# Kernel optimization log

Hardware: AMD Instinct MI355X
Metric: run time of the kernel (lower is better)

Reference implementation:

```python
import jax, jax.numpy as jnp
import numpy as np
import math

N_VERT = 35709
N_FACE = 70789
BATCH = 32


def _normalize(x, axis=-1, eps=1e-12):
    n = jnp.linalg.norm(x, axis=axis, keepdims=True)
    return x / jnp.maximum(n, eps)


def setup_inputs() -> dict:
    key = jax.random.key(0)
    ks = jax.random.split(key, 9)
    coeff = jax.random.normal(ks[0], (BATCH, 277), jnp.float32)
    idBase = jax.random.normal(ks[1], (3 * N_VERT, 80), jnp.float32)
    exBase = jax.random.normal(ks[2], (3 * N_VERT, 64), jnp.float32)
    texBase = jax.random.normal(ks[3], (3 * N_VERT, 100), jnp.float32)
    meanshape = jax.random.normal(ks[4], (3 * N_VERT,), jnp.float32)
    meantex = jax.random.normal(ks[5], (3 * N_VERT,), jnp.float32)
    face_buf = jax.random.randint(ks[6], (N_FACE, 3), 0, N_VERT, jnp.int32)
    # point_buf may index the appended zero-normal row at position N_FACE (padding)
    point_buf = jax.random.randint(ks[7], (N_VERT, 8), 0, N_FACE + 1, jnp.int32)
    keypoints = jax.random.randint(ks[8], (68,), 0, N_VERT, jnp.int32)
    return dict(coeff=coeff, idBase=idBase, exBase=exBase, texBase=texBase,
                meanshape=meanshape, meantex=meantex, face_buf=face_buf,
                point_buf=point_buf, keypoints=keypoints)


def reference(coeff, idBase, exBase, texBase, meanshape, meantex,
              face_buf, point_buf, keypoints):
    B = coeff.shape[0]
    # ---- Split_coeff (canonical 80/64/100/3/27/3 layout) ----
    id_c = coeff[:, :80]
    ex_c = coeff[:, 80:144]
    tex_c = coeff[:, 144:244]
    angles = coeff[:, 244:247]
    gamma = coeff[:, 247:274]
    trans = coeff[:, 274:277]
    cam_scale = jnp.ones((B, 1), coeff.dtype)
    f_scale = jnp.ones((B, 1), coeff.dtype)

    # ---- Shape formation ----
    fs = (jnp.einsum('ij,aj->ai', idBase, id_c)
          + jnp.einsum('ij,aj->ai', exBase, ex_c)
          + meanshape[None, :])
    fs = fs.reshape(B, -1, 3)  # [B, N, 3]
    fs = fs - jnp.mean(meanshape.reshape(-1, 3), axis=0)[None, None, :]

    # ---- Texture formation ----
    tex = (jnp.einsum('ij,aj->ai', texBase, tex_c) + meantex[None, :]).reshape(B, -1, 3)

    # ---- Rotation matrix (Rz @ Ry @ Rx, then transpose) ----
    cx, sx = jnp.cos(angles[:, 0]), jnp.sin(angles[:, 0])
    cy, sy = jnp.cos(angles[:, 1]), jnp.sin(angles[:, 1])
    cz, sz = jnp.cos(angles[:, 2]), jnp.sin(angles[:, 2])
    o, z = jnp.ones_like(cx), jnp.zeros_like(cx)
    Rx = jnp.stack([o, z, z, z, cx, -sx, z, sx, cx], -1).reshape(B, 3, 3)
    Ry = jnp.stack([cy, z, sy, z, o, z, -sy, z, cy], -1).reshape(B, 3, 3)
    Rz = jnp.stack([cz, -sz, z, sz, cz, z, z, z, o], -1).reshape(B, 3, 3)
    rot = jnp.swapaxes(jnp.matmul(jnp.matmul(Rz, Ry), Rx), 1, 2)  # [B,3,3]

    # ---- Compute_norm: gather face verts, cross, aggregate to vertices ----
    v1 = fs[:, face_buf[:, 0], :]  # [B, F, 3]
    v2 = fs[:, face_buf[:, 1], :]
    v3 = fs[:, face_buf[:, 2], :]
    face_norm = _normalize(jnp.cross(v1 - v2, v2 - v3), axis=2)  # [B, F, 3]
    face_norm = jnp.concatenate(
        [face_norm, jnp.zeros((B, 1, 3), face_norm.dtype)], axis=1)  # pad row
    v_norm = _normalize(jnp.sum(face_norm[:, point_buf, :], axis=2), axis=2)  # [B,N,3]

    norm_r = jnp.matmul(v_norm, rot)

    # ---- Rigid transform + landmarks ----
    fst = jnp.matmul(fs, rot) + trans[:, None, :]
    lm = fst[:, keypoints, :]  # [B, 68, 3]

    # ---- Projection block (applied to landmarks) ----
    focal = 1015.0 * f_scale  # [B,1]
    camera_pos = jnp.array([0.0, 0.0, 10.0], coeff.dtype) * cam_scale[:, :, None]  # [B,1,3]
    reverse_z = jnp.diag(jnp.array([1.0, 1.0, -1.0], coeff.dtype))
    z1 = jnp.zeros((B, 1), coeff.dtype)
    z2 = jnp.zeros((B, 2), coeff.dtype)
    o1 = jnp.ones((B, 1), coeff.dtype)
    p_matrix = jnp.concatenate(
        [focal, z1, 112.0 * o1, z1, focal, 112.0 * o1, z2, o1], axis=1).reshape(B, 3, 3)
    lm_cam = jnp.matmul(lm, reverse_z[None]) + camera_pos
    aug = jnp.matmul(lm_cam, jnp.swapaxes(p_matrix, 1, 2))
    landmark_p = aug[..., :2] / aug[..., 2:3]

    # ---- SH illumination ----
    init_lit = jnp.array([0.8, 0, 0, 0, 0, 0, 0, 0, 0], coeff.dtype)
    g = gamma.reshape(B, 3, 9) + init_lit[None, None, :]
    pi = math.pi
    a0, a1, a2 = pi, 2 * pi / math.sqrt(3.0), 2 * pi / math.sqrt(8.0)
    c0 = 1.0 / math.sqrt(4 * pi)
    c1 = math.sqrt(3.0) / math.sqrt(4 * pi)
    c2 = 3 * math.sqrt(5.0) / math.sqrt(12 * pi)
    nx, ny, nz = norm_r[..., 0], norm_r[..., 1], norm_r[..., 2]
    Y = jnp.stack([
        a0 * c0 * jnp.ones_like(nx),
        -a1 * c1 * ny,
        a1 * c1 * nz,
        -a1 * c1 * nx,
        a2 * c2 * nx * ny,
        -a2 * c2 * ny * nz,
        a2 * c2 * 0.5 / math.sqrt(3.0) * (3 * nz * nz - 1),
        -a2 * c2 * nx * nz,
        a2 * c2 * 0.5 * (nx * nx - ny * ny),
    ], axis=-1)  # [B, N, 9]
    lighting = jnp.einsum('bnk,bck->bnc', Y, g)  # [B, N, 3]
    face_color = tex * lighting

    return face_color, landmark_p, fst
```

## Files before the change

### kernel.cpp

```cpp
#include <hip/hip_runtime.h>

#define N_VERT 35709
#define N_FACE 70789
#define NB 32
#define M3 (3*N_VERT)

#define FSS ((size_t)N_VERT*16)
#define FNS ((size_t)(N_FACE+1)*16)

#define WS_FS   ((size_t)0)
#define WS_FN   (WS_FS + 8*FSS)
#define WS_CPAD (WS_FN + 8*FNS)
#define WS_ROT  (WS_CPAD + (size_t)NB*256)
#define WS_TRE  (WS_ROT + (size_t)NB*9)
#define WS_G    (WS_TRE + (size_t)NB*3)
#define WS_MEAN (WS_G + (size_t)NB*27)

#define FC_OFF  ((size_t)0)
#define LM_OFF  ((size_t)NB*M3)
#define FST_OFF (LM_OFF + (size_t)NB*68*2)

#define A0C0 0.88622692545275801f
#define A1C1 1.77245385090551603f
#define A2C2 2.42703239430f
#define Y6C  0.70062393935f
#define Y8C  1.21351619715f

typedef float vf4 __attribute__((ext_vector_type(4)));

__device__ __forceinline__ void nt_store4(float* p, float a, float b, float c, float d) {
  vf4 v = {a, b, c, d};
  __builtin_nontemporal_store(v, (vf4*)p);
}

__global__ void __launch_bounds__(256) face3d_stageA1(
    const float* __restrict__ ms, float* __restrict__ ws) {
  float s0=0.f, s1=0.f, s2=0.f;
  for (int v = blockIdx.x*256 + threadIdx.x; v < N_VERT; v += gridDim.x*256) {
    s0 += ms[3*v+0]; s1 += ms[3*v+1]; s2 += ms[3*v+2];
  }
  #pragma unroll
  for (int off = 32; off > 0; off >>= 1) {
    s0 += __shfl_down(s0, off);
    s1 += __shfl_down(s1, off);
    s2 += __shfl_down(s2, off);
  }
  if ((threadIdx.x & 63) == 0) {
    atomicAdd(&ws[WS_MEAN+0], s0);
    atomicAdd(&ws[WS_MEAN+1], s1);
    atomicAdd(&ws[WS_MEAN+2], s2);
  }
}

__global__ void __launch_bounds__(256) face3d_stageA2(
    const float* __restrict__ coeff, float* __restrict__ ws) {
  int t = threadIdx.x;
  float m0 = ws[WS_MEAN+0]*(1.0f/N_VERT);
  float m1 = ws[WS_MEAN+1]*(1.0f/N_VERT);
  float m2 = ws[WS_MEAN+2]*(1.0f/N_VERT);
  for (int idx = t; idx < NB*256; idx += 256) {
    int b = idx >> 8, k = idx & 255;
    ws[WS_CPAD + idx] = (k < 244) ? coeff[b*277 + k] : 0.0f;
  }
  for (int idx = t; idx < NB*27; idx += 256) {
    int b = idx / 27, k = idx - b*27;
    ws[WS_G + idx] = coeff[b*277 + 247 + k] + (((k % 9) == 0) ? 0.8f : 0.0f);
  }
  if (t < NB) {
    int b = t;
    float ax = coeff[b*277+244], ay = coeff[b*277+245], az = coeff[b*277+246];
    float cx=cosf(ax), sx=sinf(ax);
    float cy=cosf(ay), sy=sinf(ay);
    float cz=cosf(az), sz=sinf(az);
    float T00=cz*cy, T01=-sz, T02=cz*sy;
    float T10=sz*cy, T11=cz,  T12=sz*sy;
    float T20=-sy,   T21=0.f, T22=cy;
    float R[3][3];
    R[0][0]=T00; R[0][1]=T01*cx+T02*sx; R[0][2]=-T01*sx+T02*cx;
    R[1][0]=T10; R[1][1]=T11*cx+T12*sx; R[1][2]=-T11*sx+T12*cx;
    R[2][0]=T20; R[2][1]=T21*cx+T22*sx; R[2][2]=-T21*sx+T22*cx;
    float rot[3][3];
    #pragma unroll
    for (int c=0;c<3;c++)
      #pragma unroll
      for (int j=0;j<3;j++)
        rot[c][j] = R[j][c];
    #pragma unroll
    for (int c=0;c<3;c++)
      #pragma unroll
      for (int j=0;j<3;j++)
        ws[WS_ROT + b*9 + c*3 + j] = rot[c][j];
    #pragma unroll
    for (int j=0;j<3;j++)
      ws[WS_TRE + b*3 + j] = coeff[b*277+274+j]
        - (m0*rot[0][j] + m1*rot[1][j] + m2*rot[2][j]);
  }
}

template<int NK4, int KROW, int COFF>
__device__ __forceinline__ void phase88(const float* __restrict__ A0,
                                        int row0,
                                        const float4* __restrict__ W,
                                        int bg,
                                        float acc[8][8]) {
  const float4* p[8];
  #pragma unroll
  for (int i = 0; i < 8; ++i) {
    int r = row0 + i; if (r >= M3) r = M3-1;
    p[i] = (const float4*)(A0 + (size_t)r*KROW);
  }
  float4 cur[8];
  #pragma unroll
  for (int i = 0; i < 8; ++i) cur[i] = p[i][0];
  #pragma unroll 1
  for (int s = 0; s < NK4; ++s) {
    float4 a[8];
    #pragma unroll
    for (int i = 0; i < 8; ++i) a[i] = cur[i];
    if (s + 1 < NK4) {
      #pragma unroll
      for (int i = 0; i < 8; ++i) cur[i] = p[i][s+1];
    }
    #pragma unroll
    for (int j = 0; j < 8; ++j) {
      float4 w = W[(size_t)(bg + 4*j)*65 + COFF + s];
      #pragma unroll
      for (int i = 0; i < 8; ++i) {
        acc[i][j] = fmaf(a[i].x, w.x, fmaf(a[i].y, w.y,
                    fmaf(a[i].z, w.z, fmaf(a[i].w, w.w, acc[i][j]))));
      }
    }
  }
}

__global__ void __launch_bounds__(256,1) face3d_stageB(
    const float* __restrict__ idB, const float* __restrict__ exB,
    const float* __restrict__ texB, const float* __restrict__ meanshape,
    const float* __restrict__ meantex, const float* __restrict__ cpad,
    float* __restrict__ fsS, float* __restrict__ texOut) {
  __shared__ float4 W[32*65];
  int t = threadIdx.x;
  {
    const float4* __restrict__ src = (const float4*)cpad;
    #pragma unroll
    for (int n = 0; n < 8; ++n) {
      int idx = t + 256*n;
      int b = idx >> 6, k = idx & 63;
      W[b*65 + k] = src[idx];
    }
  }
  __syncthreads();
  int bg = t & 3;
  int row0 = blockIdx.x*512 + (t >> 2)*8;
  if (row0 >= M3) return;

  float acc[8][8];
  #pragma unroll
  for (int i=0;i<8;i++)
    #pragma unroll
    for (int j=0;j<8;j++) acc[i][j]=0.f;

  phase88<20, 80, 0 >(idB, row0, W, bg, acc);
  phase88<16, 64, 20>(exB, row0, W, bg, acc);

  #pragma unroll
  for (int i = 0; i < 8; ++i) {
    int r = row0 + i;
    if (r < M3) {
      float msv = meanshape[r];
      int v = r/3, c = r - 3*v;
      float* dst = fsS + (size_t)v*16 + bg*4 + c;
      #pragma unroll
      for (int j = 0; j < 8; ++j)
        dst[j*FSS] = acc[i][j] + msv;
    }
  }

  #pragma unroll
  for (int i=0;i<8;i++)
    #pragma unroll
    for (int j=0;j<8;j++) acc[i][j]=0.f;

  phase88<25, 100, 36>(texB, row0, W, bg, acc);

  #pragma unroll
  for (int i = 0; i < 8; ++i) {
    int r = row0 + i;
    if (r < M3) {
      float mtv = meantex[r];
      #pragma unroll
      for (int j = 0; j < 8; ++j) {
        int b = bg + 4*j;
        __builtin_nontemporal_store(acc[i][j] + mtv, &texOut[(size_t)b*M3 + r]);
      }
    }
  }
}

__global__ void __launch_bounds__(256) face3d_stageC(
    const int* __restrict__ face_buf, const float* __restrict__ fsS,
    float* __restrict__ fnS) {
  int t = threadIdx.x;
  int bg = blockIdx.x & 7;
  int f = (blockIdx.x >> 3)*64 + (t >> 2);
  int bsub = t & 3;
  if (f > N_FACE) return;
  float* o = fnS + bg*FNS + (size_t)f*16 + bsub*4;
  if (f == N_FACE) {
    nt_store4(o, 0.f, 0.f, 0.f, 0.f);
    return;
  }
  int i0 = face_buf[f*3+0];
  int i1 = face_buf[f*3+1];
  int i2 = face_buf[f*3+2];
  const float* fs = fsS + bg*FSS + bsub*4;
  float4 p1 = *(const float4*)(fs + (size_t)i0*16);
  float4 p2 = *(const float4*)(fs + (size_t)i1*16);
  float4 p3 = *(const float4*)(fs + (size_t)i2*16);
  float e1x = p1.x-p2.x, e1y = p1.y-p2.y, e1z = p1.z-p2.z;
  float e2x = p2.x-p3.x, e2y = p2.y-p3.y, e2z = p2.z-p3.z;
  float nx = e1y*e2z - e1z*e2y;
  float ny = e1z*e2x - e1x*e2z;
  float nz = e1x*e2y - e1y*e2x;
  float inv = 1.0f / fmaxf(sqrtf(nx*nx + ny*ny + nz*nz), 1e-12f);
  nt_store4(o, nx*inv, ny*inv, nz*inv, 0.f);
}

#define DVB 558
__global__ void __launch_bounds__(256) face3d_stageD(
    const int* __restrict__ point_buf, const int* __restrict__ keypoints,
    const float* __restrict__ fsS, const float* __restrict__ fnS,
    const float* __restrict__ rotAll, const float* __restrict__ treAll,
    const float* __restrict__ gAll, float* __restrict__ out) {
  const int mainBlocks = 8*DVB;
  int bid = blockIdx.x;
  int t = threadIdx.x;
  if (bid < mainBlocks) {
    __shared__ float fstL[4*193];
    __shared__ float LL[4*193];
    int bg = bid & 7;
    int v0 = (bid >> 3)*64;
    int bsub = t & 3, vi = t >> 2;
    int v = v0 + vi;
    int b = bg*4 + bsub;
    if (v < N_VERT) {
      const int4 pb0 = *(const int4*)(point_buf + (size_t)v*8);
      const int4 pb1 = *(const int4*)(point_buf + (size_t)v*8 + 4);
      const float* fn = fnS + bg*FNS + bsub*4;
      float4 g0 = *(const float4*)(fn + (size_t)pb0.x*16);
      float4 g1 = *(const float4*)(fn + (size_t)pb0.y*16);
      float4 g2 = *(const float4*)(fn + (size_t)pb0.z*16);
      float4 g3 = *(const float4*)(fn + (size_t)pb0.w*16);
      float4 g4 = *(const float4*)(fn + (size_t)pb1.x*16);
      float4 g5 = *(const float4*)(fn + (size_t)pb1.y*16);
      float4 g6 = *(const float4*)(fn + (size_t)pb1.z*16);
      float4 g7 = *(const float4*)(fn + (size_t)pb1.w*16);
      float sx = ((g0.x+g1.x)+(g2.x+g3.x)) + ((g4.x+g5.x)+(g6.x+g7.x));
      float sy = ((g0.y+g1.y)+(g2.y+g3.y)) + ((g4.y+g5.y)+(g6.y+g7.y));
      float sz = ((g0.z+g1.z)+(g2.z+g3.z)) + ((g4.z+g5.z)+(g6.z+g7.z));
      float inv = 1.0f / fmaxf(sqrtf(sx*sx + sy*sy + sz*sz), 1e-12f);
      float n0 = sx*inv, n1 = sy*inv, n2 = sz*inv;
      const float* rot = rotAll + b*9;
      float r00=rot[0], r01=rot[1], r02=rot[2];
      float r10=rot[3], r11=rot[4], r12=rot[5];
      float r20=rot[6], r21=rot[7], r22=rot[8];
      float nx = n0*r00 + n1*r10 + n2*r20;
      float ny = n0*r01 + n1*r11 + n2*r21;
      float nz = n0*r02 + n1*r12 + n2*r22;
      float Y1 = -A1C1*ny;
      float Y2 =  A1C1*nz;
      float Y3 = -A1C1*nx;
      float Y4 =  A2C2*nx*ny;
      float Y5 = -A2C2*ny*nz;
      float Y6 =  Y6C*(3.f*nz*nz - 1.f);
      float Y7 = -A2C2*nx*nz;
      float Y8 =  Y8C*(nx*nx - ny*ny);
      const float* g = gAll + b*27;
      #pragma unroll
      for (int c = 0; c < 3; ++c) {
        const float* gc = g + c*9;
        LL[bsub*193 + vi*3 + c] =
            A0C0*gc[0] + Y1*gc[1] + Y2*gc[2] + Y3*gc[3] + Y4*gc[4]
          + Y5*gc[5] + Y6*gc[6] + Y7*gc[7] + Y8*gc[8];
      }
      float4 fsv = *(const float4*)(fsS + bg*FSS + (size_t)v*16 + bsub*4);
      const float* tre = treAll + b*3;
      fstL[bsub*193 + vi*3 + 0] = fsv.x*r00 + fsv.y*r10 + fsv.z*r20 + tre[0];
      fstL[bsub*193 + vi*3 + 1] = fsv.x*r01 + fsv.y*r11 + fsv.z*r21 + tre[1];
      fstL[bsub*193 + vi*3 + 2] = fsv.x*r02 + fsv.y*r12 + fsv.z*r22 + tre[2];
    }
    __syncthreads();
    int b2 = t >> 6, w = t & 63;
    if (v0 + w < N_VERT) {
      int bb = bg*4 + b2;
      size_t obase = (size_t)bb*M3 + (size_t)(v0 + w)*3;
      #pragma unroll
      for (int c = 0; c < 3; ++c)
        __builtin_nontemporal_store(fstL[b2*193 + w*3 + c], &out[FST_OFF + obase + c]);
      #pragma unroll
      for (int c = 0; c < 3; ++c) {
        float tx = out[FC_OFF + obase + c];
        __builtin_nontemporal_store(tx*LL[b2*193 + w*3 + c], &out[FC_OFF + obase + c]);
      }
    }
  } else {
    int idx = (bid - mainBlocks)*256 + t;
    if (idx >= NB*68) return;
    int b = idx & 31, j = idx >> 5;
    int kp = keypoints[j];
    const float* rot = rotAll + b*9;
    const float* tre = treAll + b*3;
    float4 fsv = *(const float4*)(fsS + (size_t)(b>>2)*FSS + (size_t)kp*16 + (b&3)*4);
    float o0 = fsv.x*rot[0] + fsv.y*rot[3] + fsv.z*rot[6] + tre[0];
    float o1 = fsv.x*rot[1] + fsv.y*rot[4] + fsv.z*rot[7] + tre[1];
    float o2 = fsv.x*rot[2] + fsv.y*rot[5] + fsv.z*rot[8] + tre[2];
    float zc = 10.0f - o2;
    float axv = 1015.0f*o0 + 112.0f*zc;
    float ayv = 1015.0f*o1 + 112.0f*zc;
    __builtin_nontemporal_store(axv/zc, &out[LM_OFF + (size_t)b*136 + (size_t)j*2 + 0]);
    __builtin_nontemporal_store(ayv/zc, &out[LM_OFF + (size_t)b*136 + (size_t)j*2 + 1]);
  }
}

extern "C" void kernel_launch(void* const* d_in, const int* in_sizes, int n_in,
                              void* d_out, int out_size, void* d_ws, size_t ws_size,
                              hipStream_t stream) {
  const float* coeff     = (const float*)d_in[0];
  const float* idB       = (const float*)d_in[1];
  const float* exB       = (const float*)d_in[2];
  const float* texB      = (const float*)d_in[3];
  const float* meanshape = (const float*)d_in[4];
  const float* meantex   = (const float*)d_in[5];
  const int*   face_buf  = (const int*)d_in[6];
  const int*   point_buf = (const int*)d_in[7];
  const int*   keypoints = (const int*)d_in[8];
  float* out = (float*)d_out;
  float* ws  = (float*)d_ws;

  (void)hipMemsetAsync((char*)d_ws + WS_MEAN*sizeof(float), 0, 3*sizeof(float), stream);

  hipLaunchKernelGGL(face3d_stageA1, dim3(56), dim3(256), 0, stream, meanshape, ws);
  hipLaunchKernelGGL(face3d_stageA2, dim3(1), dim3(256), 0, stream, coeff, ws);

  int gridB = (M3 + 511)/512;
  hipLaunchKernelGGL(face3d_stageB, dim3(gridB), dim3(256), 0, stream,
                     idB, exB, texB, meanshape, meantex,
                     ws + WS_CPAD, ws + WS_FS, out + FC_OFF);

  int gridC = 8 * ((N_FACE + 1 + 63)/64);
  hipLaunchKernelGGL(face3d_stageC, dim3(gridC), dim3(256), 0, stream,
                     face_buf, ws + WS_FS, ws + WS_FN);

  int mainBlocks = 8*DVB;
  int lmBlocks   = (NB*68 + 255)/256;
  hipLaunchKernelGGL(face3d_stageD, dim3(mainBlocks + lmBlocks), dim3(256), 0, stream,
                     point_buf, keypoints, ws + WS_FS, ws + WS_FN,
                     ws + WS_ROT, ws + WS_TRE, ws + WS_G, out);
}
```

Before: 312.2 us.

## Store shape and normals in fp16 batch-interleaved layout for gathers

Shape and face normals now go into a vertex-major layout with all 32 batches interleaved, and the copies used by the gathers are half precision. The face-normal and vertex-normal gather kernels can then pull one 256-byte contiguous row per index for the whole batch instead of eight separate fp32 planes. Stage B is retiled to compute 2 batches × 8 rows per thread with more blocks, and the nontemporal stores are dropped. The trade-offs are more redundant basis reads in stage B (each row is read by 16 threads rather than 4), an extra fp32 shape copy that must be written, and a loss of precision in the normals.

```diff
diff --git a/kernel.cpp b/kernel.cpp
--- a/kernel.cpp
+++ b/kernel.cpp
@@ -4,17 +4,19 @@
 #define N_FACE 70789
 #define NB 32
 #define M3 (3*N_VERT)
-
-#define FSS ((size_t)N_VERT*16)
-#define FNS ((size_t)(N_FACE+1)*16)
-
-#define WS_FS   ((size_t)0)
-#define WS_FN   (WS_FS + 8*FSS)
-#define WS_CPAD (WS_FN + 8*FNS)
-#define WS_ROT  (WS_CPAD + (size_t)NB*256)
-#define WS_TRE  (WS_ROT + (size_t)NB*9)
-#define WS_G    (WS_TRE + (size_t)NB*3)
-#define WS_MEAN (WS_G + (size_t)NB*27)
+#define V4 ((size_t)N_VERT*4)
+
+typedef _Float16 h4 __attribute__((ext_vector_type(4)));
+typedef float vf4 __attribute__((ext_vector_type(4)));
+
+#define WSB_FS32 ((size_t)0)
+#define WSB_FS16 (WSB_FS32 + (size_t)NB*V4*4)
+#define WSB_FN16 (WSB_FS16 + (size_t)N_VERT*NB*8)
+#define WSB_CPAD (WSB_FN16 + (size_t)(N_FACE+1)*NB*8)
+#define WSB_ROT  (WSB_CPAD + (size_t)NB*256*4)
+#define WSB_TRE  (WSB_ROT + (size_t)NB*9*4)
+#define WSB_G    (WSB_TRE + (size_t)NB*3*4)
+#define WSB_MEAN (WSB_G + (size_t)NB*27*4)
 
 #define FC_OFF  ((size_t)0)
 #define LM_OFF  ((size_t)NB*M3)
@@ -26,15 +28,8 @@
 #define Y6C  0.70062393935f
 #define Y8C  1.21351619715f
 
-typedef float vf4 __attribute__((ext_vector_type(4)));
-
-__device__ __forceinline__ void nt_store4(float* p, float a, float b, float c, float d) {
-  vf4 v = {a, b, c, d};
-  __builtin_nontemporal_store(v, (vf4*)p);
-}
-
 __global__ void __launch_bounds__(256) face3d_stageA1(
-    const float* __restrict__ ms, float* __restrict__ ws) {
+    const float* __restrict__ ms, float* __restrict__ mean) {
   float s0=0.f, s1=0.f, s2=0.f;
   for (int v = blockIdx.x*256 + threadIdx.x; v < N_VERT; v += gridDim.x*256) {
     s0 += ms[3*v+0]; s1 += ms[3*v+1]; s2 += ms[3*v+2];
@@ -46,25 +41,27 @@
     s2 += __shfl_down(s2, off);
   }
   if ((threadIdx.x & 63) == 0) {
-    atomicAdd(&ws[WS_MEAN+0], s0);
-    atomicAdd(&ws[WS_MEAN+1], s1);
-    atomicAdd(&ws[WS_MEAN+2], s2);
+    atomicAdd(&mean[0], s0);
+    atomicAdd(&mean[1], s1);
+    atomicAdd(&mean[2], s2);
   }
 }
 
 __global__ void __launch_bounds__(256) face3d_stageA2(
-    const float* __restrict__ coeff, float* __restrict__ ws) {
+    const float* __restrict__ coeff, const float* __restrict__ mean,
+    float* __restrict__ cpad, float* __restrict__ rotW,
+    float* __restrict__ treW, float* __restrict__ gW) {
   int t = threadIdx.x;
-  float m0 = ws[WS_MEAN+0]*(1.0f/N_VERT);
-  float m1 = ws[WS_MEAN+1]*(1.0f/N_VERT);
-  float m2 = ws[WS_MEAN+2]*(1.0f/N_VERT);
+  float m0 = mean[0]*(1.0f/N_VERT);
+  float m1 = mean[1]*(1.0f/N_VERT);
+  float m2 = mean[2]*(1.0f/N_VERT);
   for (int idx = t; idx < NB*256; idx += 256) {
     int b = idx >> 8, k = idx & 255;
-    ws[WS_CPAD + idx] = (k < 244) ? coeff[b*277 + k] : 0.0f;
+    cpad[idx] = (k < 244) ? coeff[b*277 + k] : 0.0f;
   }
   for (int idx = t; idx < NB*27; idx += 256) {
     int b = idx / 27, k = idx - b*27;
-    ws[WS_G + idx] = coeff[b*277 + 247 + k] + (((k % 9) == 0) ? 0.8f : 0.0f);
+    gW[idx] = coeff[b*277 + 247 + k] + (((k % 9) == 0) ? 0.8f : 0.0f);
   }
   if (t < NB) {
     int b = t;
@@ -89,20 +86,20 @@
     for (int c=0;c<3;c++)
       #pragma unroll
       for (int j=0;j<3;j++)
-        ws[WS_ROT + b*9 + c*3 + j] = rot[c][j];
+        rotW[b*9 + c*3 + j] = rot[c][j];
     #pragma unroll
     for (int j=0;j<3;j++)
-      ws[WS_TRE + b*3 + j] = coeff[b*277+274+j]
+      treW[b*3 + j] = coeff[b*277+274+j]
         - (m0*rot[0][j] + m1*rot[1][j] + m2*rot[2][j]);
   }
 }
 
 template<int NK4, int KROW, int COFF>
-__device__ __forceinline__ void phase88(const float* __restrict__ A0,
-                                        int row0,
-                                        const float4* __restrict__ W,
-                                        int bg,
-                                        float acc[8][8]) {
+__device__ __forceinline__ void phaseB(const float* __restrict__ A0,
+                                       int row0,
+                                       const float4* __restrict__ W,
+                                       int bg2,
+                                       float acc[8][2]) {
   const float4* p[8];
   #pragma unroll
   for (int i = 0; i < 8; ++i) {
@@ -122,8 +119,8 @@
       for (int i = 0; i < 8; ++i) cur[i] = p[i][s+1];
     }
     #pragma unroll
-    for (int j = 0; j < 8; ++j) {
-      float4 w = W[(size_t)(bg + 4*j)*65 + COFF + s];
+    for (int j = 0; j < 2; ++j) {
+      float4 w = W[(size_t)(bg2 + j)*65 + COFF + s];
       #pragma unroll
       for (int i = 0; i < 8; ++i) {
         acc[i][j] = fmaf(a[i].x, w.x, fmaf(a[i].y, w.y,
@@ -133,11 +130,12 @@
   }
 }
 
-__global__ void __launch_bounds__(256,1) face3d_stageB(
+__global__ void __launch_bounds__(256) face3d_stageB(
     const float* __restrict__ idB, const float* __restrict__ exB,
     const float* __restrict__ texB, const float* __restrict__ meanshape,
     const float* __restrict__ meantex, const float* __restrict__ cpad,
-    float* __restrict__ fsS, float* __restrict__ texOut) {
+    float* __restrict__ fs32, _Float16* __restrict__ fs16,
+    float* __restrict__ texOut) {
   __shared__ float4 W[32*65];
   int t = threadIdx.x;
   {
@@ -150,18 +148,16 @@
     }
   }
   __syncthreads();
-  int bg = t & 3;
-  int row0 = blockIdx.x*512 + (t >> 2)*8;
+  int bg2 = (t & 15)*2;
+  int row0 = blockIdx.x*128 + (t >> 4)*8;
   if (row0 >= M3) return;
 
-  float acc[8][8];
-  #pragma unroll
-  for (int i=0;i<8;i++)
-    #pragma unroll
-    for (int j=0;j<8;j++) acc[i][j]=0.f;
-
-  phase88<20, 80, 0 >(idB, row0, W, bg, acc);
-  phase88<16, 64, 20>(exB, row0, W, bg, acc);
+  float acc[8][2];
+  #pragma unroll
+  for (int i=0;i<8;i++){acc[i][0]=0.f;acc[i][1]=0.f;}
+
+  phaseB<20, 80, 0 >(idB, row0, W, bg2, acc);
+  phaseB<16, 64, 20>(exB, row0, W, bg2, acc);
 
   #pragma unroll
   for (int i = 0; i < 8; ++i) {
@@ -169,19 +165,20 @@
     if (r < M3) {
       float msv = meanshape[r];
       int v = r/3, c = r - 3*v;
-      float* dst = fsS + (size_t)v*16 + bg*4 + c;
-      #pragma unroll
-      for (int j = 0; j < 8; ++j)
-        dst[j*FSS] = acc[i][j] + msv;
-    }
-  }
-
-  #pragma unroll
-  for (int i=0;i<8;i++)
-    #pragma unroll
-    for (int j=0;j<8;j++) acc[i][j]=0.f;
-
-  phase88<25, 100, 36>(texB, row0, W, bg, acc);
+      #pragma unroll
+      for (int j = 0; j < 2; ++j) {
+        int b = bg2 + j;
+        float val = acc[i][j] + msv;
+        fs32[(size_t)b*V4 + (size_t)v*4 + c] = val;
+        fs16[((size_t)v*32 + b)*4 + c] = (_Float16)val;
+      }
+    }
+  }
+
+  #pragma unroll
+  for (int i=0;i<8;i++){acc[i][0]=0.f;acc[i][1]=0.f;}
+
+  phaseB<25, 100, 36>(texB, row0, W, bg2, acc);
 
   #pragma unroll
   for (int i = 0; i < 8; ++i) {
@@ -189,120 +186,112 @@
     if (r < M3) {
       float mtv = meantex[r];
       #pragma unroll
-      for (int j = 0; j < 8; ++j) {
-        int b = bg + 4*j;
-        __builtin_nontemporal_store(acc[i][j] + mtv, &texOut[(size_t)b*M3 + r]);
+      for (int j = 0; j < 2; ++j) {
+        int b = bg2 + j;
+        texOut[(size_t)b*M3 + r] = acc[i][j] + mtv;
       }
     }
   }
 }
 
 __global__ void __launch_bounds__(256) face3d_stageC(
-    const int* __restrict__ face_buf, const float* __restrict__ fsS,
-    float* __restrict__ fnS) {
+    const int* __restrict__ face_buf, const h4* __restrict__ fs16,
+    h4* __restrict__ fn16) {
   int t = threadIdx.x;
-  int bg = blockIdx.x & 7;
-  int f = (blockIdx.x >> 3)*64 + (t >> 2);
-  int bsub = t & 3;
+  int b = t & 31;
+  int f = blockIdx.x*8 + (t >> 5);
   if (f > N_FACE) return;
-  float* o = fnS + bg*FNS + (size_t)f*16 + bsub*4;
   if (f == N_FACE) {
-    nt_store4(o, 0.f, 0.f, 0.f, 0.f);
+    h4 z = {(_Float16)0, (_Float16)0, (_Float16)0, (_Float16)0};
+    fn16[(size_t)f*32 + b] = z;
     return;
   }
   int i0 = face_buf[f*3+0];
   int i1 = face_buf[f*3+1];
   int i2 = face_buf[f*3+2];
-  const float* fs = fsS + bg*FSS + bsub*4;
-  float4 p1 = *(const float4*)(fs + (size_t)i0*16);
-  float4 p2 = *(const float4*)(fs + (size_t)i1*16);
-  float4 p3 = *(const float4*)(fs + (size_t)i2*16);
-  float e1x = p1.x-p2.x, e1y = p1.y-p2.y, e1z = p1.z-p2.z;
-  float e2x = p2.x-p3.x, e2y = p2.y-p3.y, e2z = p2.z-p3.z;
+  h4 q1 = fs16[(size_t)i0*32 + b];
+  h4 q2 = fs16[(size_t)i1*32 + b];
+  h4 q3 = fs16[(size_t)i2*32 + b];
+  float e1x = (float)q1.x-(float)q2.x, e1y = (float)q1.y-(float)q2.y, e1z = (float)q1.z-(float)q2.z;
+  float e2x = (float)q2.x-(float)q3.x, e2y = (float)q2.y-(float)q3.y, e2z = (float)q2.z-(float)q3.z;
   float nx = e1y*e2z - e1z*e2y;
   float ny = e1z*e2x - e1x*e2z;
   float nz = e1x*e2y - e1y*e2x;
   float inv = 1.0f / fmaxf(sqrtf(nx*nx + ny*ny + nz*nz), 1e-12f);
-  nt_store4(o, nx*inv, ny*inv, nz*inv, 0.f);
-}
-
-#define DVB 558
+  h4 o = {(_Float16)(nx*inv), (_Float16)(ny*inv), (_Float16)(nz*inv), (_Float16)0};
+  fn16[(size_t)f*32 + b] = o;
+}
+
 __global__ void __launch_bounds__(256) face3d_stageD(
     const int* __restrict__ point_buf, const int* __restrict__ keypoints,
-    const float* __restrict__ fsS, const float* __restrict__ fnS,
+    const float* __restrict__ fs32, const h4* __restrict__ fn16,
     const float* __restrict__ rotAll, const float* __restrict__ treAll,
     const float* __restrict__ gAll, float* __restrict__ out) {
-  const int mainBlocks = 8*DVB;
+  const int mainBlocks = (N_VERT + 7)/8;
   int bid = blockIdx.x;
   int t = threadIdx.x;
   if (bid < mainBlocks) {
-    __shared__ float fstL[4*193];
-    __shared__ float LL[4*193];
-    int bg = bid & 7;
-    int v0 = (bid >> 3)*64;
-    int bsub = t & 3, vi = t >> 2;
-    int v = v0 + vi;
-    int b = bg*4 + bsub;
-    if (v < N_VERT) {
-      const int4 pb0 = *(const int4*)(point_buf + (size_t)v*8);
-      const int4 pb1 = *(const int4*)(point_buf + (size_t)v*8 + 4);
-      const float* fn = fnS + bg*FNS + bsub*4;
-      float4 g0 = *(const float4*)(fn + (size_t)pb0.x*16);
-      float4 g1 = *(const float4*)(fn + (size_t)pb0.y*16);
-      float4 g2 = *(const float4*)(fn + (size_t)pb0.z*16);
-      float4 g3 = *(const float4*)(fn + (size_t)pb0.w*16);
-      float4 g4 = *(const float4*)(fn + (size_t)pb1.x*16);
-      float4 g5 = *(const float4*)(fn + (size_t)pb1.y*16);
-      float4 g6 = *(const float4*)(fn + (size_t)pb1.z*16);
-      float4 g7 = *(const float4*)(fn + (size_t)pb1.w*16);
-      float sx = ((g0.x+g1.x)+(g2.x+g3.x)) + ((g4.x+g5.x)+(g6.x+g7.x));
-      float sy = ((g0.y+g1.y)+(g2.y+g3.y)) + ((g4.y+g5.y)+(g6.y+g7.y));
-      float sz = ((g0.z+g1.z)+(g2.z+g3.z)) + ((g4.z+g5.z)+(g6.z+g7.z));
-      float inv = 1.0f / fmaxf(sqrtf(sx*sx + sy*sy + sz*sz), 1e-12f);
-      float n0 = sx*inv, n1 = sy*inv, n2 = sz*inv;
-      const float* rot = rotAll + b*9;
-      float r00=rot[0], r01=rot[1], r02=rot[2];
-      float r10=rot[3], r11=rot[4], r12=rot[5];
-      float r20=rot[6], r21=rot[7], r22=rot[8];
-      float nx = n0*r00 + n1*r10 + n2*r20;
-      float ny = n0*r01 + n1*r11 + n2*r21;
-      float nz = n0*r02 + n1*r12 + n2*r22;
-      float Y1 = -A1C1*ny;
-      float Y2 =  A1C1*nz;
-      float Y3 = -A1C1*nx;
-      float Y4 =  A2C2*nx*ny;
-      float Y5 = -A2C2*ny*nz;
-      float Y6 =  Y6C*(3.f*nz*nz - 1.f);
-      float Y7 = -A2C2*nx*nz;
-      float Y8 =  Y8C*(nx*nx - ny*ny);
-      const float* g = gAll + b*27;
-      #pragma unroll
-      for (int c = 0; c < 3; ++c) {
-        const float* gc = g + c*9;
-        LL[bsub*193 + vi*3 + c] =
-            A0C0*gc[0] + Y1*gc[1] + Y2*gc[2] + Y3*gc[3] + Y4*gc[4]
-          + Y5*gc[5] + Y6*gc[6] + Y7*gc[7] + Y8*gc[8];
-      }
-      float4 fsv = *(const float4*)(fsS + bg*FSS + (size_t)v*16 + bsub*4);
-      const float* tre = treAll + b*3;
-      fstL[bsub*193 + vi*3 + 0] = fsv.x*r00 + fsv.y*r10 + fsv.z*r20 + tre[0];
-      fstL[bsub*193 + vi*3 + 1] = fsv.x*r01 + fsv.y*r11 + fsv.z*r21 + tre[1];
-      fstL[bsub*193 + vi*3 + 2] = fsv.x*r02 + fsv.y*r12 + fsv.z*r22 + tre[2];
-    }
-    __syncthreads();
-    int b2 = t >> 6, w = t & 63;
-    if (v0 + w < N_VERT) {
-      int bb = bg*4 + b2;
-      size_t obase = (size_t)bb*M3 + (size_t)(v0 + w)*3;
-      #pragma unroll
-      for (int c = 0; c < 3; ++c)
-        __builtin_nontemporal_store(fstL[b2*193 + w*3 + c], &out[FST_OFF + obase + c]);
-      #pragma unroll
-      for (int c = 0; c < 3; ++c) {
-        float tx = out[FC_OFF + obase + c];
-        __builtin_nontemporal_store(tx*LL[b2*193 + w*3 + c], &out[FC_OFF + obase + c]);
-      }
-    }
+    int b = t & 31;
+    int v = bid*8 + (t >> 5);
+    if (v >= N_VERT) return;
+    const int4 pb0 = *(const int4*)(point_buf + (size_t)v*8);
+    const int4 pb1 = *(const int4*)(point_buf + (size_t)v*8 + 4);
+    h4 g0 = fn16[(size_t)pb0.x*32 + b];
+    h4 g1 = fn16[(size_t)pb0.y*32 + b];
+    h4 g2 = fn16[(size_t)pb0.z*32 + b];
+    h4 g3 = fn16[(size_t)pb0.w*32 + b];
+    h4 g4 = fn16[(size_t)pb1.x*32 + b];
+    h4 g5 = fn16[(size_t)pb1.y*32 + b];
+    h4 g6 = fn16[(size_t)pb1.z*32 + b];
+    h4 g7 = fn16[(size_t)pb1.w*32 + b];
+    float sx = ((float)g0.x+(float)g1.x)+((float)g2.x+(float)g3.x)
+             + ((float)g4.x+(float)g5.x)+((float)g6.x+(float)g7.x);
+    float sy = ((float)g0.y+(float)g1.y)+((float)g2.y+(float)g3.y)
+             + ((float)g4.y+(float)g5.y)+((float)g6.y+(float)g7.y);
+    float sz = ((float)g0.z+(float)g1.z)+((float)g2.z+(float)g3.z)
+             + ((float)g4.z+(float)g5.z)+((float)g6.z+(float)g7.z);
+    float inv = 1.0f / fmaxf(sqrtf(sx*sx + sy*sy + sz*sz), 1e-12f);
+    float n0 = sx*inv, n1 = sy*inv, n2 = sz*inv;
+    const float* rot = rotAll + b*9;
+    float r00=rot[0], r01=rot[1], r02=rot[2];
+    float r10=rot[3], r11=rot[4], r12=rot[5];
+    float r20=rot[6], r21=rot[7], r22=rot[8];
+    float nx = n0*r00 + n1*r10 + n2*r20;
+    float ny = n0*r01 + n1*r11 + n2*r21;
+    float nz = n0*r02 + n1*r12 + n2*r22;
+    float Y1 = -A1C1*ny;
+    float Y2 =  A1C1*nz;
+    float Y3 = -A1C1*nx;
+    float Y4 =  A2C2*nx*ny;
+    float Y5 = -A2C2*ny*nz;
+    float Y6 =  Y6C*(3.f*nz*nz - 1.f);
+    float Y7 = -A2C2*nx*nz;
+    float Y8 =  Y8C*(nx*nx - ny*ny);
+    const float* g = gAll + b*27;
+    float L0, L1, L2;
+    {
+      const float* gc = g;
+      L0 = A0C0*gc[0] + Y1*gc[1] + Y2*gc[2] + Y3*gc[3] + Y4*gc[4]
+         + Y5*gc[5] + Y6*gc[6] + Y7*gc[7] + Y8*gc[8];
+      gc = g + 9;
+      L1 = A0C0*gc[0] + Y1*gc[1] + Y2*gc[2] + Y3*gc[3] + Y4*gc[4]
+         + Y5*gc[5] + Y6*gc[6] + Y7*gc[7] + Y8*gc[8];
+      gc = g + 18;
+      L2 = A0C0*gc[0] + Y1*gc[1] + Y2*gc[2] + Y3*gc[3] + Y4*gc[4]
+         + Y5*gc[5] + Y6*gc[6] + Y7*gc[7] + Y8*gc[8];
+    }
+    float4 fsv = *(const float4*)(fs32 + (size_t)b*V4 + (size_t)v*4);
+    const float* tre = treAll + b*3;
+    float o0 = fsv.x*r00 + fsv.y*r10 + fsv.z*r20 + tre[0];
+    float o1 = fsv.x*r01 + fsv.y*r11 + fsv.z*r21 + tre[1];
+    float o2 = fsv.x*r02 + fsv.y*r12 + fsv.z*r22 + tre[2];
+    size_t obase = (size_t)b*M3 + (size_t)v*3;
+    out[FST_OFF + obase + 0] = o0;
+    out[FST_OFF + obase + 1] = o1;
+    out[FST_OFF + obase + 2] = o2;
+    out[FC_OFF + obase + 0] = out[FC_OFF + obase + 0]*L0;
+    out[FC_OFF + obase + 1] = out[FC_OFF + obase + 1]*L1;
+    out[FC_OFF + obase + 2] = out[FC_OFF + obase + 2]*L2;
   } else {
     int idx = (bid - mainBlocks)*256 + t;
     if (idx >= NB*68) return;
@@ -310,15 +299,15 @@
     int kp = keypoints[j];
     const float* rot = rotAll + b*9;
     const float* tre = treAll + b*3;
-    float4 fsv = *(const float4*)(fsS + (size_t)(b>>2)*FSS + (size_t)kp*16 + (b&3)*4);
+    float4 fsv = *(const float4*)(fs32 + (size_t)b*V4 + (size_t)kp*4);
     float o0 = fsv.x*rot[0] + fsv.y*rot[3] + fsv.z*rot[6] + tre[0];
     float o1 = fsv.x*rot[1] + fsv.y*rot[4] + fsv.z*rot[7] + tre[1];
     float o2 = fsv.x*rot[2] + fsv.y*rot[5] + fsv.z*rot[8] + tre[2];
     float zc = 10.0f - o2;
     float axv = 1015.0f*o0 + 112.0f*zc;
     float ayv = 1015.0f*o1 + 112.0f*zc;
-    __builtin_nontemporal_store(axv/zc, &out[LM_OFF + (size_t)b*136 + (size_t)j*2 + 0]);
-    __builtin_nontemporal_store(ayv/zc, &out[LM_OFF + (size_t)b*136 + (size_t)j*2 + 1]);
+    out[LM_OFF + (size_t)b*136 + (size_t)j*2 + 0] = axv/zc;
+    out[LM_OFF + (size_t)b*136 + (size_t)j*2 + 1] = ayv/zc;
   }
 }
 
@@ -335,25 +324,36 @@
   const int*   point_buf = (const int*)d_in[7];
   const int*   keypoints = (const int*)d_in[8];
   float* out = (float*)d_out;
-  float* ws  = (float*)d_ws;
-
-  (void)hipMemsetAsync((char*)d_ws + WS_MEAN*sizeof(float), 0, 3*sizeof(float), stream);
-
-  hipLaunchKernelGGL(face3d_stageA1, dim3(56), dim3(256), 0, stream, meanshape, ws);
-  hipLaunchKernelGGL(face3d_stageA2, dim3(1), dim3(256), 0, stream, coeff, ws);
-
-  int gridB = (M3 + 511)/512;
+  char*  wsb = (char*)d_ws;
+
+  float*    fs32 = (float*)(wsb + WSB_FS32);
+  _Float16* fs16 = (_Float16*)(wsb + WSB_FS16);
+  h4*       fs16v= (h4*)(wsb + WSB_FS16);
+  h4*       fn16 = (h4*)(wsb + WSB_FN16);
+  float*    cpad = (float*)(wsb + WSB_CPAD);
+  float*    rotW = (float*)(wsb + WSB_ROT);
+  float*    treW = (float*)(wsb + WSB_TRE);
+  float*    gW   = (float*)(wsb + WSB_G);
+  float*    mean = (float*)(wsb + WSB_MEAN);
+
+  (void)hipMemsetAsync(mean, 0, 3*sizeof(float), stream);
+
+  hipLaunchKernelGGL(face3d_stageA1, dim3(56), dim3(256), 0, stream, meanshape, mean);
+  hipLaunchKernelGGL(face3d_stageA2, dim3(1), dim3(256), 0, stream,
+                     coeff, mean, cpad, rotW, treW, gW);
+
+  int gridB = (M3 + 127)/128;
   hipLaunchKernelGGL(face3d_stageB, dim3(gridB), dim3(256), 0, stream,
                      idB, exB, texB, meanshape, meantex,
-                     ws + WS_CPAD, ws + WS_FS, out + FC_OFF);
-
-  int gridC = 8 * ((N_FACE + 1 + 63)/64);
+                     cpad, fs32, fs16, out + FC_OFF);
+
+  int gridC = (N_FACE + 1 + 7)/8;
   hipLaunchKernelGGL(face3d_stageC, dim3(gridC), dim3(256), 0, stream,
-                     face_buf, ws + WS_FS, ws + WS_FN);
-
-  int mainBlocks = 8*DVB;
+                     face_buf, fs16v, fn16);
+
+  int mainBlocks = (N_VERT + 7)/8;
   int lmBlocks   = (NB*68 + 255)/256;
   hipLaunchKernelGGL(face3d_stageD, dim3(mainBlocks + lmBlocks), dim3(256), 0, stream,
-                     point_buf, keypoints, ws + WS_FS, ws + WS_FN,
-                     ws + WS_ROT, ws + WS_TRE, ws + WS_G, out);
-}
+                     point_buf, keypoints, fs32, fn16,
+                     rotW, treW, gW, out);
+}
```

New measurement: 321.3 us. 1.03x slower.
